# Performance work log

Measured on AMD Instinct MI355X. Metric: run time of the kernel, lower is better.

## Reference

```python
import jax, jax.numpy as jnp
import numpy as np

NUM_BINS = 64
TMIN, TMAX = 0.0, 1.0
SMIN, SMAX = 0.0, 1.0
BW_T = (TMAX - TMIN) / NUM_BINS
BW_S = (SMAX - SMIN) / NUM_BINS
EPS_T = 1.0 * BW_T
EPS_S = 1.0 * BW_S


def _cubic_bspline(x):
    t = jnp.abs(x)
    inner = 2.0 / 3.0 - t * t + 0.5 * t * t * t          # |x| < 1
    outer = ((2.0 - t) ** 3) / 6.0                        # 1 <= |x| < 2
    return jnp.where(t < 1.0, inner, jnp.where(t < 2.0, outer, 0.0))


def _normalise_minmax(x, min_out, max_out):
    # x: (N, L); per-sample minmax normalisation
    x_min = jnp.min(x, axis=1, keepdims=True)
    x_max = jnp.max(x, axis=1, keepdims=True)
    return (x - x_min) / (x_max - x_min + 1e-12) * (max_out - min_out) + min_out


def setup_inputs() -> dict:
    key = jax.random.key(0)
    k1, k2 = jax.random.split(key)
    target = jax.random.uniform(k1, (4, 1, 64, 64, 64), dtype=jnp.float32)
    source = jax.random.uniform(k2, (4, 1, 64, 64, 64), dtype=jnp.float32)
    return {"target": target, "source": source}


def reference(target, source):
    N = target.shape[0]
    t = _normalise_minmax(target[:, 0].reshape(N, -1), TMIN, TMAX)  # (N, L)
    s = _normalise_minmax(source[:, 0].reshape(N, -1), SMIN, SMAX)  # (N, L)

    bins_t = (jnp.arange(NUM_BINS, dtype=jnp.float32) * BW_T + TMIN)  # (B,)
    bins_s = (jnp.arange(NUM_BINS, dtype=jnp.float32) * BW_S + SMIN)  # (B,)

    # (N, B, L)
    D_t = (bins_t[None, :, None] - t[:, None, :]) / EPS_T
    D_s = (bins_s[None, :, None] - s[:, None, :]) / EPS_S
    W_t = _cubic_bspline(D_t)
    W_s = _cubic_bspline(D_s)

    # joint histogram: (N, B, B)
    hist_joint = jnp.einsum('nil,njl->nij', W_t, W_s) / (EPS_T * EPS_S)

    hist_norm = jnp.sum(hist_joint, axis=(1, 2))                      # (N,)
    p_joint = hist_joint / hist_norm[:, None, None]
    p_target = jnp.sum(p_joint, axis=2)                                # (N, B)
    p_source = jnp.sum(p_joint, axis=1)                                # (N, B)

    ent_target = -jnp.sum(p_target * jnp.log(p_target + 1e-12), axis=1)
    ent_source = -jnp.sum(p_source * jnp.log(p_source + 1e-12), axis=1)
    ent_joint = -jnp.sum(p_joint * jnp.log(p_joint + 1e-12), axis=(1, 2))

    # nmi=True branch
    return -jnp.mean((ent_target + ent_source) / ent_joint)
```

## Files before the change

### kernel.cpp

```cpp
#include <hip/hip_runtime.h>
#include <math.h>

#define NSAMP 4
#define NB 64
#define LVOL (64*64*64)
#define WPS 128
#define PADR 68
#define KBLK 8
#define TILEB (PADR*64)
#define ABYTES (KBLK*TILEB)
#define SWZ(a,row) ((a) ^ ((((row)>>1)&7)<<4))

typedef __attribute__((ext_vector_type(8))) short bf16x8;
typedef __attribute__((ext_vector_type(4))) float f32x4;

__device__ __forceinline__ unsigned short f2bf(float x){
  unsigned u = __float_as_uint(x);
  return (unsigned short)((u + 0x7FFFu + ((u >> 16) & 1u)) >> 16);
}

__global__ __launch_bounds__(256) void k_minmax(const float* __restrict__ tgt,
                                                const float* __restrict__ src,
                                                float4* __restrict__ mmp,
                                                int* __restrict__ cnt){
  const int n = blockIdx.x >> 6, chunk = blockIdx.x & 63;
  if (blockIdx.x == 0 && threadIdx.x < 8) cnt[threadIdx.x] = 0;
  const float4* t4 = (const float4*)(tgt + (size_t)n * LVOL) + (size_t)chunk * 1024;
  const float4* s4 = (const float4*)(src + (size_t)n * LVOL) + (size_t)chunk * 1024;
  float tmn = INFINITY, tmx = -INFINITY, smn = INFINITY, smx = -INFINITY;
  #pragma unroll
  for (int i = 0; i < 4; ++i){
    float4 a = t4[threadIdx.x + i * 256];
    tmn = fminf(tmn, fminf(fminf(a.x, a.y), fminf(a.z, a.w)));
    tmx = fmaxf(tmx, fmaxf(fmaxf(a.x, a.y), fmaxf(a.z, a.w)));
    float4 b = s4[threadIdx.x + i * 256];
    smn = fminf(smn, fminf(fminf(b.x, b.y), fminf(b.z, b.w)));
    smx = fmaxf(smx, fmaxf(fmaxf(b.x, b.y), fmaxf(b.z, b.w)));
  }
  for (int off = 32; off; off >>= 1){
    tmn = fminf(tmn, __shfl_down(tmn, off));
    tmx = fmaxf(tmx, __shfl_down(tmx, off));
    smn = fminf(smn, __shfl_down(smn, off));
    smx = fmaxf(smx, __shfl_down(smx, off));
  }
  __shared__ float red[4][4];
  const int wave = threadIdx.x >> 6, lane = threadIdx.x & 63;
  if (lane == 0){ red[wave][0]=tmn; red[wave][1]=tmx; red[wave][2]=smn; red[wave][3]=smx; }
  __syncthreads();
  if (threadIdx.x == 0){
    for (int w = 1; w < 4; ++w){
      tmn = fminf(tmn, red[w][0]); tmx = fmaxf(tmx, red[w][1]);
      smn = fminf(smn, red[w][2]); smx = fmaxf(smx, red[w][3]);
    }
    mmp[blockIdx.x] = make_float4(tmn, tmx, smn, smx);
  }
}

__global__ __launch_bounds__(256, 2) void k_hist(const float* __restrict__ tgt,
                                                 const float* __restrict__ src,
                                                 const float4* __restrict__ mmp,
                                                 float* __restrict__ P){
  __shared__ __align__(16) char lds[2 * ABYTES];
  __shared__ float mmsh[4];
  const int tid = threadIdx.x;
  const int n = blockIdx.x >> 7, wg = blockIdx.x & (WPS - 1);
  if (tid < 64){
    float4 v = mmp[n * 64 + tid];
    for (int off = 32; off; off >>= 1){
      v.x = fminf(v.x, __shfl_down(v.x, off));
      v.y = fmaxf(v.y, __shfl_down(v.y, off));
      v.z = fminf(v.z, __shfl_down(v.z, off));
      v.w = fmaxf(v.w, __shfl_down(v.w, off));
    }
    if (tid == 0){ mmsh[0]=v.x; mmsh[1]=v.y; mmsh[2]=v.z; mmsh[3]=v.w; }
  }
  {
    int4 zz = make_int4(0, 0, 0, 0);
    #pragma unroll
    for (int i = 0; i < 17; ++i) ((int4*)lds)[tid + i * 256] = zz;
  }
  __syncthreads();
  const float tmn = mmsh[0], smn = mmsh[2];
  const float st = (float)NB / (mmsh[1] - tmn + 1e-12f);
  const float ss = (float)NB / (mmsh[3] - smn + 1e-12f);
  const size_t vbase = (size_t)n * LVOL + (size_t)wg * 2048;
  const int kb_ = tid >> 5, k2 = tid & 31;
  const int lane = tid & 63, wv = tid >> 6;
  const int r = lane & 15, g = lane >> 4;
  const int rb = 32 * (wv >> 1), cb = 32 * (wv & 1);
  int sa[2], sb[2];
  #pragma unroll
  for (int ai = 0; ai < 2; ++ai){
    int ar = 1 + rb + 16 * ai + r;
    sa[ai] = SWZ(ar * 64 + g * 16, ar);
  }
  #pragma unroll
  for (int bj = 0; bj < 2; ++bj){
    int br = 1 + cb + 16 * bj + r;
    sb[bj] = ABYTES + SWZ(br * 64 + g * 16, br);
  }
  f32x4 acc[2][2];
  #pragma unroll
  for (int ai = 0; ai < 2; ++ai)
    #pragma unroll
    for (int bj = 0; bj < 2; ++bj) acc[ai][bj] = (f32x4){0.f, 0.f, 0.f, 0.f};

  const int baseT = kb_ * TILEB + k2 * 2;
  const int baseS = ABYTES + baseT;
  int piu_t = 0, piu_s = 0;
  for (int it = 0; it < 8; ++it){
    __syncthreads();
    if (it){
      #pragma unroll
      for (int a = 0; a < 4; ++a){
        int rt = piu_t + a, rs = piu_s + a;
        *(unsigned short*)(lds + SWZ(baseT + rt * 64, rt)) = 0;
        *(unsigned short*)(lds + SWZ(baseS + rs * 64, rs)) = 0;
      }
    }
    const float tv = tgt[vbase + (size_t)it * 256 + tid];
    const float sv = src[vbase + (size_t)it * 256 + tid];
    {
      float u = (tv - tmn) * st;
      float fu = floorf(u); int iu = (int)fu; float f = u - fu, q = 1.f - f;
      float w0 = q*q*q*(1.f/6.f), w3 = f*f*f*(1.f/6.f);
      float w1 = (2.f/3.f) - f*f + 0.5f*f*f*f, w2 = 1.f - w0 - w1 - w3;
      float w[4] = {w0, w1, w2, w3};
      piu_t = iu;
      #pragma unroll
      for (int a = 0; a < 4; ++a){
        int row = iu + a;
        *(unsigned short*)(lds + SWZ(baseT + row * 64, row)) = f2bf(w[a]);
      }
    }
    {
      float u = (sv - smn) * ss;
      float fu = floorf(u); int iu = (int)fu; float f = u - fu, q = 1.f - f;
      float w0 = q*q*q*(1.f/6.f), w3 = f*f*f*(1.f/6.f);
      float w1 = (2.f/3.f) - f*f + 0.5f*f*f*f, w2 = 1.f - w0 - w1 - w3;
      float w[4] = {w0, w1, w2, w3};
      piu_s = iu;
      #pragma unroll
      for (int a = 0; a < 4; ++a){
        int row = iu + a;
        *(unsigned short*)(lds + SWZ(baseS + row * 64, row)) = f2bf(w[a]);
      }
    }
    __syncthreads();
    #pragma unroll
    for (int kb = 0; kb < KBLK; ++kb){
      const char* p = lds + kb * TILEB;
      bf16x8 a0 = *(const bf16x8*)(p + sa[0]);
      bf16x8 a1 = *(const bf16x8*)(p + sa[1]);
      bf16x8 b0 = *(const bf16x8*)(p + sb[0]);
      bf16x8 b1 = *(const bf16x8*)(p + sb[1]);
      acc[0][0] = __builtin_amdgcn_mfma_f32_16x16x32_bf16(a0, b0, acc[0][0], 0, 0, 0);
      acc[0][1] = __builtin_amdgcn_mfma_f32_16x16x32_bf16(a0, b1, acc[0][1], 0, 0, 0);
      acc[1][0] = __builtin_amdgcn_mfma_f32_16x16x32_bf16(a1, b0, acc[1][0], 0, 0, 0);
      acc[1][1] = __builtin_amdgcn_mfma_f32_16x16x32_bf16(a1, b1, acc[1][1], 0, 0, 0);
    }
  }
  float* Pp = P + (size_t)blockIdx.x * 4096;
  #pragma unroll
  for (int ai = 0; ai < 2; ++ai)
    #pragma unroll
    for (int bj = 0; bj < 2; ++bj)
      #pragma unroll
      for (int e = 0; e < 4; ++e)
        Pp[(rb + 16 * ai + g * 4 + e) * 64 + cb + 16 * bj + r] = acc[ai][bj][e];
}

__global__ __launch_bounds__(256) void k_finish(const float* __restrict__ P,
                                                float* __restrict__ hist,
                                                float* __restrict__ ratio,
                                                int* __restrict__ cnt,
                                                float* __restrict__ out){
  __shared__ float4 sh4[4][64];
  __shared__ int flag;
  __shared__ float rowsum[NB], colsum[NB], wr1[4], wr2[4], S_sh;
  const int tid = threadIdx.x;
  const int n = blockIdx.x >> 4, c = blockIdx.x & 15;
  {
    const int f4 = tid & 63, wrange = tid >> 6;
    const float4* P4 = (const float4*)P;
    size_t base = ((size_t)n * WPS + (size_t)wrange * 32) * 1024 + c * 64 + f4;
    float4 acc = make_float4(0.f, 0.f, 0.f, 0.f);
    for (int w = 0; w < 32; ++w){
      float4 v = P4[base + (size_t)w * 1024];
      acc.x += v.x; acc.y += v.y; acc.z += v.z; acc.w += v.w;
    }
    sh4[wrange][f4] = acc;
    __syncthreads();
    if (tid < 64){
      float4 a = sh4[0][tid], b = sh4[1][tid], d = sh4[2][tid], e = sh4[3][tid];
      float4 s;
      s.x = a.x + b.x + d.x + e.x; s.y = a.y + b.y + d.y + e.y;
      s.z = a.z + b.z + d.z + e.z; s.w = a.w + b.w + d.w + e.w;
      ((float4*)hist)[(size_t)n * 1024 + c * 64 + tid] = s;
    }
  }
  __threadfence();
  __syncthreads();
  if (tid == 0) flag = atomicAdd(&cnt[n], 1);
  __syncthreads();
  if (flag != 15) return;
  __threadfence();
  float* h = hist + n * 4096;
  if (tid < NB){ rowsum[tid] = 0.f; colsum[tid] = 0.f; }
  __syncthreads();
  const int rr = tid >> 2, c0 = (tid & 3) * 16;
  float hv[16];
  float rsum = 0.f;
  #pragma unroll
  for (int k = 0; k < 16; ++k){
    hv[k] = atomicAdd(&h[rr * 64 + c0 + k], 0.f);
    rsum += hv[k];
  }
  atomicAdd(&rowsum[rr], rsum);
  #pragma unroll
  for (int k = 0; k < 16; ++k) atomicAdd(&colsum[c0 + k], hv[k]);
  float part = rsum;
  for (int off = 32; off; off >>= 1) part += __shfl_down(part, off);
  if ((tid & 63) == 0) wr1[tid >> 6] = part;
  __syncthreads();
  if (tid == 0) S_sh = wr1[0] + wr1[1] + wr1[2] + wr1[3];
  __syncthreads();
  const float invS = 1.f / S_sh;
  float ej = 0.f;
  #pragma unroll
  for (int k = 0; k < 16; ++k){
    float p = hv[k] * invS;
    ej -= p * logf(p + 1e-12f);
  }
  for (int off = 32; off; off >>= 1) ej += __shfl_down(ej, off);
  if ((tid & 63) == 0) wr2[tid >> 6] = ej;
  float em = 0.f;
  if (tid < NB){
    float pt = rowsum[tid] * invS;
    float ps = colsum[tid] * invS;
    em = -pt * logf(pt + 1e-12f) - ps * logf(ps + 1e-12f);
    for (int off = 32; off; off >>= 1) em += __shfl_down(em, off);
  }
  __syncthreads();
  if (tid == 0){
    float EJ = wr2[0] + wr2[1] + wr2[2] + wr2[3];
    ratio[n] = em / EJ;
    __threadfence();
    int f2 = atomicAdd(&cnt[4], 1);
    if (f2 == 3){
      __threadfence();
      float s = 0.f;
      #pragma unroll
      for (int m = 0; m < NSAMP; ++m) s += atomicAdd(&ratio[m], 0.f);
      out[0] = -0.25f * s;
    }
  }
}

extern "C" void kernel_launch(void* const* d_in, const int* in_sizes, int n_in,
                              void* d_out, int out_size, void* d_ws, size_t ws_size,
                              hipStream_t stream){
  const float* tgt = (const float*)d_in[0];
  const float* src = (const float*)d_in[1];
  float* out = (float*)d_out;
  char* ws = (char*)d_ws;
  float4* mmp = (float4*)ws;
  int*   cnt  = (int*)(ws + 4096);
  float* ratio= (float*)(ws + 4352);
  float* hist = (float*)(ws + 4608);
  float* P    = (float*)(ws + 73728);
  k_minmax<<<NSAMP * 64, 256, 0, stream>>>(tgt, src, mmp, cnt);
  k_hist  <<<NSAMP * WPS, 256, 0, stream>>>(tgt, src, mmp, P);
  k_finish<<<NSAMP * 16, 256, 0, stream>>>(P, hist, ratio, cnt, out);
}
```

Before: 49.51 us.

## Fuse finish into hist kernel with per-wave private tiles and last-block reduction

Each wave now builds its own bf16 weight tiles and computes the full 64x64 partial histogram with 16 MFMA accumulators, which removes the block-wide barriers inside the sample loop. The four wave partials are summed through LDS before one store per block. The separate finish kernel is folded in: the last 16 blocks per sample to finish reduce the per-block partials, and the final block computes the entropies. This saves a kernel launch and the per-iteration syncs, but adds atomic counter handshakes, more accumulator registers, and a serial 128-way reduction done by only 16 blocks.

```diff
diff --git a/kernel.cpp b/kernel.cpp
--- a/kernel.cpp
+++ b/kernel.cpp
@@ -5,10 +5,9 @@
 #define NB 64
 #define LVOL (64*64*64)
 #define WPS 128
-#define PADR 68
-#define KBLK 8
-#define TILEB (PADR*64)
-#define ABYTES (KBLK*TILEB)
+#define NFIN 16
+#define TILEB (68*64)
+#define WTILE (4*TILEB)
 #define SWZ(a,row) ((a) ^ ((((row)>>1)&7)<<4))
 
 typedef __attribute__((ext_vector_type(8))) short bf16x8;
@@ -23,8 +22,8 @@
                                                 const float* __restrict__ src,
                                                 float4* __restrict__ mmp,
                                                 int* __restrict__ cnt){
+  if (blockIdx.x == 0 && threadIdx.x < 16) cnt[threadIdx.x] = 0;
   const int n = blockIdx.x >> 6, chunk = blockIdx.x & 63;
-  if (blockIdx.x == 0 && threadIdx.x < 8) cnt[threadIdx.x] = 0;
   const float4* t4 = (const float4*)(tgt + (size_t)n * LVOL) + (size_t)chunk * 1024;
   const float4* s4 = (const float4*)(src + (size_t)n * LVOL) + (size_t)chunk * 1024;
   float tmn = INFINITY, tmx = -INFINITY, smn = INFINITY, smx = -INFINITY;
@@ -56,70 +55,68 @@
   }
 }
 
-__global__ __launch_bounds__(256, 2) void k_hist(const float* __restrict__ tgt,
-                                                 const float* __restrict__ src,
-                                                 const float4* __restrict__ mmp,
-                                                 float* __restrict__ P){
-  __shared__ __align__(16) char lds[2 * ABYTES];
-  __shared__ float mmsh[4];
-  const int tid = threadIdx.x;
+__global__ __launch_bounds__(256) void k_hist(const float* __restrict__ tgt,
+                                              const float* __restrict__ src,
+                                              const float4* __restrict__ mmp,
+                                              float* __restrict__ P,
+                                              float* __restrict__ hist,
+                                              float* __restrict__ ratio,
+                                              int* __restrict__ cnt,
+                                              float* __restrict__ out){
+  __shared__ __align__(16) char lds[4 * WTILE];
+  __shared__ int fl;
+  __shared__ float rowsum[NB], colsum[NB], wr1[4], wr2[4], S_sh;
+  const int tid = threadIdx.x, wv = tid >> 6, lane = tid & 63;
   const int n = blockIdx.x >> 7, wg = blockIdx.x & (WPS - 1);
-  if (tid < 64){
-    float4 v = mmp[n * 64 + tid];
-    for (int off = 32; off; off >>= 1){
-      v.x = fminf(v.x, __shfl_down(v.x, off));
-      v.y = fmaxf(v.y, __shfl_down(v.y, off));
-      v.z = fminf(v.z, __shfl_down(v.z, off));
-      v.w = fmaxf(v.w, __shfl_down(v.w, off));
-    }
-    if (tid == 0){ mmsh[0]=v.x; mmsh[1]=v.y; mmsh[2]=v.z; mmsh[3]=v.w; }
-  }
+
+  float4 v = mmp[n * 64 + lane];
+  for (int off = 32; off; off >>= 1){
+    v.x = fminf(v.x, __shfl_down(v.x, off));
+    v.y = fmaxf(v.y, __shfl_down(v.y, off));
+    v.z = fminf(v.z, __shfl_down(v.z, off));
+    v.w = fmaxf(v.w, __shfl_down(v.w, off));
+  }
+  const float tmn = __shfl(v.x, 0), tmx = __shfl(v.y, 0);
+  const float smn = __shfl(v.z, 0), smx = __shfl(v.w, 0);
+  const float st = (float)NB / (tmx - tmn + 1e-12f);
+  const float ss = (float)NB / (smx - smn + 1e-12f);
+
+  char* wt = lds + wv * WTILE;
   {
     int4 zz = make_int4(0, 0, 0, 0);
     #pragma unroll
-    for (int i = 0; i < 17; ++i) ((int4*)lds)[tid + i * 256] = zz;
-  }
-  __syncthreads();
-  const float tmn = mmsh[0], smn = mmsh[2];
-  const float st = (float)NB / (mmsh[1] - tmn + 1e-12f);
-  const float ss = (float)NB / (mmsh[3] - smn + 1e-12f);
-  const size_t vbase = (size_t)n * LVOL + (size_t)wg * 2048;
-  const int kb_ = tid >> 5, k2 = tid & 31;
-  const int lane = tid & 63, wv = tid >> 6;
+    for (int i = 0; i < 17; ++i) ((int4*)wt)[lane + i * 64] = zz;
+  }
+  const size_t vbase = (size_t)n * LVOL + (size_t)wg * 2048 + (size_t)wv * 512;
+  const int kb_w = lane >> 5, k2 = lane & 31;
+  const int baseT = kb_w * TILEB + k2 * 2;
+  const int baseS = 2 * TILEB + baseT;
   const int r = lane & 15, g = lane >> 4;
-  const int rb = 32 * (wv >> 1), cb = 32 * (wv & 1);
-  int sa[2], sb[2];
-  #pragma unroll
-  for (int ai = 0; ai < 2; ++ai){
-    int ar = 1 + rb + 16 * ai + r;
-    sa[ai] = SWZ(ar * 64 + g * 16, ar);
-  }
-  #pragma unroll
-  for (int bj = 0; bj < 2; ++bj){
-    int br = 1 + cb + 16 * bj + r;
-    sb[bj] = ABYTES + SWZ(br * 64 + g * 16, br);
-  }
-  f32x4 acc[2][2];
-  #pragma unroll
-  for (int ai = 0; ai < 2; ++ai)
-    #pragma unroll
-    for (int bj = 0; bj < 2; ++bj) acc[ai][bj] = (f32x4){0.f, 0.f, 0.f, 0.f};
-
-  const int baseT = kb_ * TILEB + k2 * 2;
-  const int baseS = ABYTES + baseT;
+  int sa[4], sb[4];
+  #pragma unroll
+  for (int i = 0; i < 4; ++i){
+    int row = 1 + 16 * i + r;
+    sa[i] = SWZ(row * 64 + g * 16, row);
+    sb[i] = 2 * TILEB + sa[i];
+  }
+  f32x4 acc[4][4];
+  #pragma unroll
+  for (int ai = 0; ai < 4; ++ai)
+    #pragma unroll
+    for (int bj = 0; bj < 4; ++bj) acc[ai][bj] = (f32x4){0.f, 0.f, 0.f, 0.f};
+
   int piu_t = 0, piu_s = 0;
   for (int it = 0; it < 8; ++it){
-    __syncthreads();
     if (it){
       #pragma unroll
       for (int a = 0; a < 4; ++a){
         int rt = piu_t + a, rs = piu_s + a;
-        *(unsigned short*)(lds + SWZ(baseT + rt * 64, rt)) = 0;
-        *(unsigned short*)(lds + SWZ(baseS + rs * 64, rs)) = 0;
+        *(unsigned short*)(wt + SWZ(baseT + rt * 64, rt)) = 0;
+        *(unsigned short*)(wt + SWZ(baseS + rs * 64, rs)) = 0;
       }
     }
-    const float tv = tgt[vbase + (size_t)it * 256 + tid];
-    const float sv = src[vbase + (size_t)it * 256 + tid];
+    const float tv = tgt[vbase + it * 64 + lane];
+    const float sv = src[vbase + it * 64 + lane];
     {
       float u = (tv - tmn) * st;
       float fu = floorf(u); int iu = (int)fu; float f = u - fu, q = 1.f - f;
@@ -130,7 +127,7 @@
       #pragma unroll
       for (int a = 0; a < 4; ++a){
         int row = iu + a;
-        *(unsigned short*)(lds + SWZ(baseT + row * 64, row)) = f2bf(w[a]);
+        *(unsigned short*)(wt + SWZ(baseT + row * 64, row)) = f2bf(w[a]);
       }
     }
     {
@@ -143,68 +140,70 @@
       #pragma unroll
       for (int a = 0; a < 4; ++a){
         int row = iu + a;
-        *(unsigned short*)(lds + SWZ(baseS + row * 64, row)) = f2bf(w[a]);
+        *(unsigned short*)(wt + SWZ(baseS + row * 64, row)) = f2bf(w[a]);
       }
     }
-    __syncthreads();
-    #pragma unroll
-    for (int kb = 0; kb < KBLK; ++kb){
-      const char* p = lds + kb * TILEB;
-      bf16x8 a0 = *(const bf16x8*)(p + sa[0]);
-      bf16x8 a1 = *(const bf16x8*)(p + sa[1]);
-      bf16x8 b0 = *(const bf16x8*)(p + sb[0]);
-      bf16x8 b1 = *(const bf16x8*)(p + sb[1]);
-      acc[0][0] = __builtin_amdgcn_mfma_f32_16x16x32_bf16(a0, b0, acc[0][0], 0, 0, 0);
-      acc[0][1] = __builtin_amdgcn_mfma_f32_16x16x32_bf16(a0, b1, acc[0][1], 0, 0, 0);
-      acc[1][0] = __builtin_amdgcn_mfma_f32_16x16x32_bf16(a1, b0, acc[1][0], 0, 0, 0);
-      acc[1][1] = __builtin_amdgcn_mfma_f32_16x16x32_bf16(a1, b1, acc[1][1], 0, 0, 0);
-    }
-  }
-  float* Pp = P + (size_t)blockIdx.x * 4096;
-  #pragma unroll
-  for (int ai = 0; ai < 2; ++ai)
-    #pragma unroll
-    for (int bj = 0; bj < 2; ++bj)
-      #pragma unroll
-      for (int e = 0; e < 4; ++e)
-        Pp[(rb + 16 * ai + g * 4 + e) * 64 + cb + 16 * bj + r] = acc[ai][bj][e];
-}
-
-__global__ __launch_bounds__(256) void k_finish(const float* __restrict__ P,
-                                                float* __restrict__ hist,
-                                                float* __restrict__ ratio,
-                                                int* __restrict__ cnt,
-                                                float* __restrict__ out){
-  __shared__ float4 sh4[4][64];
-  __shared__ int flag;
-  __shared__ float rowsum[NB], colsum[NB], wr1[4], wr2[4], S_sh;
-  const int tid = threadIdx.x;
-  const int n = blockIdx.x >> 4, c = blockIdx.x & 15;
-  {
-    const int f4 = tid & 63, wrange = tid >> 6;
-    const float4* P4 = (const float4*)P;
-    size_t base = ((size_t)n * WPS + (size_t)wrange * 32) * 1024 + c * 64 + f4;
-    float4 acc = make_float4(0.f, 0.f, 0.f, 0.f);
-    for (int w = 0; w < 32; ++w){
-      float4 v = P4[base + (size_t)w * 1024];
-      acc.x += v.x; acc.y += v.y; acc.z += v.z; acc.w += v.w;
-    }
-    sh4[wrange][f4] = acc;
-    __syncthreads();
-    if (tid < 64){
-      float4 a = sh4[0][tid], b = sh4[1][tid], d = sh4[2][tid], e = sh4[3][tid];
-      float4 s;
-      s.x = a.x + b.x + d.x + e.x; s.y = a.y + b.y + d.y + e.y;
-      s.z = a.z + b.z + d.z + e.z; s.w = a.w + b.w + d.w + e.w;
-      ((float4*)hist)[(size_t)n * 1024 + c * 64 + tid] = s;
-    }
-  }
-  __threadfence();
-  __syncthreads();
-  if (tid == 0) flag = atomicAdd(&cnt[n], 1);
-  __syncthreads();
-  if (flag != 15) return;
-  __threadfence();
+    #pragma unroll
+    for (int kb = 0; kb < 2; ++kb){
+      const char* p = wt + kb * TILEB;
+      bf16x8 af[4], bfr[4];
+      #pragma unroll
+      for (int i = 0; i < 4; ++i) af[i]  = *(const bf16x8*)(p + sa[i]);
+      #pragma unroll
+      for (int i = 0; i < 4; ++i) bfr[i] = *(const bf16x8*)(p + sb[i]);
+      #pragma unroll
+      for (int ai = 0; ai < 4; ++ai)
+        #pragma unroll
+        for (int bj = 0; bj < 4; ++bj)
+          acc[ai][bj] = __builtin_amdgcn_mfma_f32_16x16x32_bf16(af[ai], bfr[bj], acc[ai][bj], 0, 0, 0);
+    }
+  }
+
+  {
+    float* wf = (float*)wt;
+    #pragma unroll
+    for (int ai = 0; ai < 4; ++ai)
+      #pragma unroll
+      for (int bj = 0; bj < 4; ++bj)
+        #pragma unroll
+        for (int e = 0; e < 4; ++e)
+          wf[(16 * ai + g * 4 + e) * 65 + 16 * bj + r] = acc[ai][bj][e];
+  }
+  __syncthreads();
+  {
+    float* Pp = P + (size_t)blockIdx.x * 4096;
+    #pragma unroll
+    for (int j = 0; j < 16; ++j){
+      int idx = j * 256 + tid;
+      int rr = idx >> 6, cc = idx & 63;
+      float s = ((const float*)(lds + 0 * WTILE))[rr * 65 + cc]
+              + ((const float*)(lds + 1 * WTILE))[rr * 65 + cc]
+              + ((const float*)(lds + 2 * WTILE))[rr * 65 + cc]
+              + ((const float*)(lds + 3 * WTILE))[rr * 65 + cc];
+      __hip_atomic_store(&Pp[idx], s, __ATOMIC_RELAXED, __HIP_MEMORY_SCOPE_AGENT);
+    }
+  }
+  __threadfence();
+  if (tid == 0) fl = atomicAdd(&cnt[n], 1);
+  __syncthreads();
+  const int f = fl;
+  if (f < WPS - NFIN) return;
+  __threadfence();
+
+  const int bin = (f - (WPS - NFIN)) * 256 + tid;
+  {
+    float* Pn = P + (size_t)n * WPS * 4096;
+    float s = 0.f;
+    for (int w = 0; w < WPS; ++w)
+      s += __hip_atomic_load(&Pn[(size_t)w * 4096 + bin], __ATOMIC_RELAXED, __HIP_MEMORY_SCOPE_AGENT);
+    __hip_atomic_store(&hist[n * 4096 + bin], s, __ATOMIC_RELAXED, __HIP_MEMORY_SCOPE_AGENT);
+  }
+  __threadfence();
+  if (tid == 0) fl = atomicAdd(&cnt[NSAMP + n], 1);
+  __syncthreads();
+  if (fl != NFIN - 1) return;
+  __threadfence();
+
   float* h = hist + n * 4096;
   if (tid < NB){ rowsum[tid] = 0.f; colsum[tid] = 0.f; }
   __syncthreads();
@@ -213,7 +212,7 @@
   float rsum = 0.f;
   #pragma unroll
   for (int k = 0; k < 16; ++k){
-    hv[k] = atomicAdd(&h[rr * 64 + c0 + k], 0.f);
+    hv[k] = __hip_atomic_load(&h[rr * 64 + c0 + k], __ATOMIC_RELAXED, __HIP_MEMORY_SCOPE_AGENT);
     rsum += hv[k];
   }
   atomicAdd(&rowsum[rr], rsum);
@@ -244,14 +243,15 @@
   __syncthreads();
   if (tid == 0){
     float EJ = wr2[0] + wr2[1] + wr2[2] + wr2[3];
-    ratio[n] = em / EJ;
+    __hip_atomic_store(&ratio[n], em / EJ, __ATOMIC_RELAXED, __HIP_MEMORY_SCOPE_AGENT);
     __threadfence();
-    int f2 = atomicAdd(&cnt[4], 1);
-    if (f2 == 3){
+    int f2 = atomicAdd(&cnt[8], 1);
+    if (f2 == NSAMP - 1){
       __threadfence();
       float s = 0.f;
       #pragma unroll
-      for (int m = 0; m < NSAMP; ++m) s += atomicAdd(&ratio[m], 0.f);
+      for (int m = 0; m < NSAMP; ++m)
+        s += __hip_atomic_load(&ratio[m], __ATOMIC_RELAXED, __HIP_MEMORY_SCOPE_AGENT);
       out[0] = -0.25f * s;
     }
   }
@@ -270,6 +270,5 @@
   float* hist = (float*)(ws + 4608);
   float* P    = (float*)(ws + 73728);
   k_minmax<<<NSAMP * 64, 256, 0, stream>>>(tgt, src, mmp, cnt);
-  k_hist  <<<NSAMP * WPS, 256, 0, stream>>>(tgt, src, mmp, P);
-  k_finish<<<NSAMP * 16, 256, 0, stream>>>(P, hist, ratio, cnt, out);
-}
+  k_hist  <<<NSAMP * WPS, 256, 0, stream>>>(tgt, src, mmp, P, hist, ratio, cnt, out);
+}
```

Result: slower. 105.4 us (+112.9%).

## Halve LDS tile per block, split target/source across waves, double block count

Applied to the files above, without the earlier changes.

Each block now stages only 4 K-slices instead of 8. Half of the threads build the target weights and the other half the source weights, so one iteration covers 128 voxels with one global load per thread. This halves LDS use, lets occupancy rise to 4 blocks per CU, and allows 256 blocks per sample when the workspace is large enough. The min/max broadcast now uses wave shuffles instead of shared memory plus a barrier. In exchange there are more synchronisation rounds per voxel, and k_finish has more partial histograms to reduce.

```diff
diff --git a/kernel.cpp b/kernel.cpp
--- a/kernel.cpp
+++ b/kernel.cpp
@@ -4,11 +4,10 @@
 #define NSAMP 4
 #define NB 64
 #define LVOL (64*64*64)
-#define WPS 128
-#define PADR 68
-#define KBLK 8
-#define TILEB (PADR*64)
-#define ABYTES (KBLK*TILEB)
+#define TILEB (68*64)
+#define KBLK 4
+#define AREG (KBLK*TILEB)
+#define LDSB (2*AREG)
 #define SWZ(a,row) ((a) ^ ((((row)>>1)&7)<<4))
 
 typedef __attribute__((ext_vector_type(8))) short bf16x8;
@@ -23,8 +22,8 @@
                                                 const float* __restrict__ src,
                                                 float4* __restrict__ mmp,
                                                 int* __restrict__ cnt){
+  if (blockIdx.x == 0 && threadIdx.x < 8) cnt[threadIdx.x] = 0;
   const int n = blockIdx.x >> 6, chunk = blockIdx.x & 63;
-  if (blockIdx.x == 0 && threadIdx.x < 8) cnt[threadIdx.x] = 0;
   const float4* t4 = (const float4*)(tgt + (size_t)n * LVOL) + (size_t)chunk * 1024;
   const float4* s4 = (const float4*)(src + (size_t)n * LVOL) + (size_t)chunk * 1024;
   float tmn = INFINITY, tmx = -INFINITY, smn = INFINITY, smx = -INFINITY;
@@ -56,48 +55,53 @@
   }
 }
 
-__global__ __launch_bounds__(256, 2) void k_hist(const float* __restrict__ tgt,
+__global__ __launch_bounds__(256, 4) void k_hist(const float* __restrict__ tgt,
                                                  const float* __restrict__ src,
                                                  const float4* __restrict__ mmp,
-                                                 float* __restrict__ P){
-  __shared__ __align__(16) char lds[2 * ABYTES];
-  __shared__ float mmsh[4];
-  const int tid = threadIdx.x;
-  const int n = blockIdx.x >> 7, wg = blockIdx.x & (WPS - 1);
-  if (tid < 64){
-    float4 v = mmp[n * 64 + tid];
-    for (int off = 32; off; off >>= 1){
-      v.x = fminf(v.x, __shfl_down(v.x, off));
-      v.y = fmaxf(v.y, __shfl_down(v.y, off));
-      v.z = fminf(v.z, __shfl_down(v.z, off));
-      v.w = fmaxf(v.w, __shfl_down(v.w, off));
-    }
-    if (tid == 0){ mmsh[0]=v.x; mmsh[1]=v.y; mmsh[2]=v.z; mmsh[3]=v.w; }
-  }
+                                                 float* __restrict__ P,
+                                                 int wpsl, int vper, int iters){
+  __shared__ __align__(16) char lds[LDSB];
+  const int tid = threadIdx.x, wv = tid >> 6, lane = tid & 63;
+  const int n = blockIdx.x >> wpsl, wg = blockIdx.x & ((1 << wpsl) - 1);
+
+  float4 v = mmp[n * 64 + lane];
+  for (int off = 32; off; off >>= 1){
+    v.x = fminf(v.x, __shfl_down(v.x, off));
+    v.y = fmaxf(v.y, __shfl_down(v.y, off));
+    v.z = fminf(v.z, __shfl_down(v.z, off));
+    v.w = fmaxf(v.w, __shfl_down(v.w, off));
+  }
+  const float tmn = __shfl(v.x, 0), tmx = __shfl(v.y, 0);
+  const float smn = __shfl(v.z, 0), smx = __shfl(v.w, 0);
+  const float st = (float)NB / (tmx - tmn + 1e-12f);
+  const float ss = (float)NB / (smx - smn + 1e-12f);
+
   {
     int4 zz = make_int4(0, 0, 0, 0);
     #pragma unroll
-    for (int i = 0; i < 17; ++i) ((int4*)lds)[tid + i * 256] = zz;
-  }
-  __syncthreads();
-  const float tmn = mmsh[0], smn = mmsh[2];
-  const float st = (float)NB / (mmsh[1] - tmn + 1e-12f);
-  const float ss = (float)NB / (mmsh[3] - smn + 1e-12f);
-  const size_t vbase = (size_t)n * LVOL + (size_t)wg * 2048;
-  const int kb_ = tid >> 5, k2 = tid & 31;
-  const int lane = tid & 63, wv = tid >> 6;
+    for (int i = 0; i < 9; ++i){
+      int idx = tid + i * 256;
+      if (idx < LDSB / 16) ((int4*)lds)[idx] = zz;
+    }
+  }
+
+  const int half = tid >> 7, v7 = tid & 127;
+  const int kb_w = v7 >> 5, k2 = v7 & 31;
+  const int sbase = half * AREG + kb_w * TILEB + k2 * 2;
+  const float mn = half ? smn : tmn;
+  const float sc = half ? ss : st;
+  const float* gsrc = half ? src : tgt;
+  const size_t gbase = (size_t)n * LVOL + (size_t)wg * vper + v7;
+
   const int r = lane & 15, g = lane >> 4;
   const int rb = 32 * (wv >> 1), cb = 32 * (wv & 1);
   int sa[2], sb[2];
   #pragma unroll
-  for (int ai = 0; ai < 2; ++ai){
-    int ar = 1 + rb + 16 * ai + r;
-    sa[ai] = SWZ(ar * 64 + g * 16, ar);
-  }
-  #pragma unroll
-  for (int bj = 0; bj < 2; ++bj){
-    int br = 1 + cb + 16 * bj + r;
-    sb[bj] = ABYTES + SWZ(br * 64 + g * 16, br);
+  for (int i = 0; i < 2; ++i){
+    int ar = 1 + rb + 16 * i + r;
+    sa[i] = SWZ(ar * 64 + g * 16, ar);
+    int br = 1 + cb + 16 * i + r;
+    sb[i] = AREG + SWZ(br * 64 + g * 16, br);
   }
   f32x4 acc[2][2];
   #pragma unroll
@@ -105,45 +109,28 @@
     #pragma unroll
     for (int bj = 0; bj < 2; ++bj) acc[ai][bj] = (f32x4){0.f, 0.f, 0.f, 0.f};
 
-  const int baseT = kb_ * TILEB + k2 * 2;
-  const int baseS = ABYTES + baseT;
-  int piu_t = 0, piu_s = 0;
-  for (int it = 0; it < 8; ++it){
+  int piu = 0;
+  for (int it = 0; it < iters; ++it){
     __syncthreads();
     if (it){
       #pragma unroll
       for (int a = 0; a < 4; ++a){
-        int rt = piu_t + a, rs = piu_s + a;
-        *(unsigned short*)(lds + SWZ(baseT + rt * 64, rt)) = 0;
-        *(unsigned short*)(lds + SWZ(baseS + rs * 64, rs)) = 0;
+        int row = piu + a;
+        *(unsigned short*)(lds + SWZ(sbase + row * 64, row)) = 0;
       }
     }
-    const float tv = tgt[vbase + (size_t)it * 256 + tid];
-    const float sv = src[vbase + (size_t)it * 256 + tid];
+    const float val = gsrc[gbase + (size_t)it * 128];
     {
-      float u = (tv - tmn) * st;
+      float u = (val - mn) * sc;
       float fu = floorf(u); int iu = (int)fu; float f = u - fu, q = 1.f - f;
       float w0 = q*q*q*(1.f/6.f), w3 = f*f*f*(1.f/6.f);
       float w1 = (2.f/3.f) - f*f + 0.5f*f*f*f, w2 = 1.f - w0 - w1 - w3;
       float w[4] = {w0, w1, w2, w3};
-      piu_t = iu;
+      piu = iu;
       #pragma unroll
       for (int a = 0; a < 4; ++a){
         int row = iu + a;
-        *(unsigned short*)(lds + SWZ(baseT + row * 64, row)) = f2bf(w[a]);
-      }
-    }
-    {
-      float u = (sv - smn) * ss;
-      float fu = floorf(u); int iu = (int)fu; float f = u - fu, q = 1.f - f;
-      float w0 = q*q*q*(1.f/6.f), w3 = f*f*f*(1.f/6.f);
-      float w1 = (2.f/3.f) - f*f + 0.5f*f*f*f, w2 = 1.f - w0 - w1 - w3;
-      float w[4] = {w0, w1, w2, w3};
-      piu_s = iu;
-      #pragma unroll
-      for (int a = 0; a < 4; ++a){
-        int row = iu + a;
-        *(unsigned short*)(lds + SWZ(baseS + row * 64, row)) = f2bf(w[a]);
+        *(unsigned short*)(lds + SWZ(sbase + row * 64, row)) = f2bf(w[a]);
       }
     }
     __syncthreads();
@@ -174,20 +161,21 @@
                                                 float* __restrict__ hist,
                                                 float* __restrict__ ratio,
                                                 int* __restrict__ cnt,
-                                                float* __restrict__ out){
+                                                float* __restrict__ out, int wps){
   __shared__ float4 sh4[4][64];
   __shared__ int flag;
   __shared__ float rowsum[NB], colsum[NB], wr1[4], wr2[4], S_sh;
   const int tid = threadIdx.x;
   const int n = blockIdx.x >> 4, c = blockIdx.x & 15;
+  const int per = wps >> 2;
   {
     const int f4 = tid & 63, wrange = tid >> 6;
     const float4* P4 = (const float4*)P;
-    size_t base = ((size_t)n * WPS + (size_t)wrange * 32) * 1024 + c * 64 + f4;
+    size_t base = ((size_t)n * wps + (size_t)wrange * per) * 1024 + c * 64 + f4;
     float4 acc = make_float4(0.f, 0.f, 0.f, 0.f);
-    for (int w = 0; w < 32; ++w){
-      float4 v = P4[base + (size_t)w * 1024];
-      acc.x += v.x; acc.y += v.y; acc.z += v.z; acc.w += v.w;
+    for (int w = 0; w < per; ++w){
+      float4 vv = P4[base + (size_t)w * 1024];
+      acc.x += vv.x; acc.y += vv.y; acc.z += vv.z; acc.w += vv.w;
     }
     sh4[wrange][f4] = acc;
     __syncthreads();
@@ -247,7 +235,7 @@
     ratio[n] = em / EJ;
     __threadfence();
     int f2 = atomicAdd(&cnt[4], 1);
-    if (f2 == 3){
+    if (f2 == NSAMP - 1){
       __threadfence();
       float s = 0.f;
       #pragma unroll
@@ -269,7 +257,12 @@
   float* ratio= (float*)(ws + 4352);
   float* hist = (float*)(ws + 4608);
   float* P    = (float*)(ws + 73728);
+  const size_t need256 = 73728ull + (size_t)NSAMP * 256 * 4096 * 4;
+  const int wps  = (ws_size >= need256) ? 256 : 128;
+  const int wpsl = (wps == 256) ? 8 : 7;
+  const int vper = LVOL / wps;
+  const int iters = vper / 128;
   k_minmax<<<NSAMP * 64, 256, 0, stream>>>(tgt, src, mmp, cnt);
-  k_hist  <<<NSAMP * WPS, 256, 0, stream>>>(tgt, src, mmp, P);
-  k_finish<<<NSAMP * 16, 256, 0, stream>>>(P, hist, ratio, cnt, out);
-}
+  k_hist  <<<NSAMP * wps, 256, 0, stream>>>(tgt, src, mmp, P, wpsl, vper, iters);
+  k_finish<<<NSAMP * 16, 256, 0, stream>>>(P, hist, ratio, cnt, out, wps);
+}
```

Result: slower. 69.00 us (+39.4%).
